# Optimization experiments

Hardware: AMD Instinct MI355X
Metric: run time of the kernel (lower is better)

## Reference

```python
import jax, jax.numpy as jnp
import numpy as np

B, S, V, CTX, NC, D, NH, L, FF, MAXS = 8, 512, 32000, 8, 512, 256, 4, 4, 512, 512
PAD = 0  # ram_model.pad_token_id


def setup_inputs() -> dict:
    key = jax.random.key(0)
    ks = iter(jax.random.split(key, 64))
    def p(shape, s=0.02):
        return jax.random.normal(next(ks), shape, jnp.float32) * s
    inp = {}
    inp["token_ids"] = jax.random.randint(next(ks), (B, S), 0, V)
    inp["ram_table"] = p((V, NC), 0.1)          # frozen RAM per-cluster scores
    inp["proj_W"] = p((NC, D)); inp["proj_b"] = jnp.zeros((D,), jnp.float32)
    inp["pos_emb"] = p((MAXS, D))
    for pre in ("sa", "ca"):
        for nm in ("Wq", "Wk", "Wv", "Wo"):
            inp[f"{pre}_{nm}"] = p((L, D, D))
        for nm in ("bq", "bk", "bv", "bo"):
            inp[f"{pre}_{nm}"] = jnp.zeros((L, D), jnp.float32)
    for i in (1, 2, 3):
        inp[f"ln{i}_s"] = jnp.ones((L, D), jnp.float32)
        inp[f"ln{i}_b"] = jnp.zeros((L, D), jnp.float32)
    inp["ff_W1"] = p((L, D, FF)); inp["ff_b1"] = jnp.zeros((L, FF), jnp.float32)
    inp["ff_W2"] = p((L, FF, D)); inp["ff_b2"] = jnp.zeros((L, D), jnp.float32)
    inp["out_W"] = p((D, V)); inp["out_b"] = jnp.zeros((V,), jnp.float32)
    return inp


def _ln(x, s, b):
    m = x.mean(-1, keepdims=True)
    v = ((x - m) ** 2).mean(-1, keepdims=True)
    return (x - m) * jax.lax.rsqrt(v + 1e-5) * s + b


def _mha(q_in, k_in, v_in, Wq, bq, Wk, bk, Wv, bv, Wo, bo, mask):
    b, sq, d = q_in.shape
    hd = d // NH
    q = (q_in @ Wq + bq).reshape(b, sq, NH, hd)
    k = (k_in @ Wk + bk).reshape(b, -1, NH, hd)
    v = (v_in @ Wv + bv).reshape(b, -1, NH, hd)
    sc = jnp.einsum("bqhd,bkhd->bhqk", q, k) / np.sqrt(hd).astype(np.float32)
    if mask is not None:
        sc = jnp.where(mask, -1e9, sc)  # mask broadcast over [b, h]
    a = jax.nn.softmax(sc, axis=-1)
    o = jnp.einsum("bhqk,bkhd->bqhd", a, v).reshape(b, sq, d)
    return o @ Wo + bo


def _forward(token_ids, ram_table, proj_W, proj_b, pos_emb,
             sa_Wq, sa_bq, sa_Wk, sa_bk, sa_Wv, sa_bv, sa_Wo, sa_bo,
             ca_Wq, ca_bq, ca_Wk, ca_bk, ca_Wv, ca_bv, ca_Wo, ca_bo,
             ln1_s, ln1_b, ln2_s, ln2_b, ln3_s, ln3_b,
             ff_W1, ff_b1, ff_W2, ff_b2, out_W, out_b):
    b, s = token_ids.shape
    # Batched sliding context windows (replaces the per-position Python loop):
    # left-pad with PAD so window at pos covers [pos-CTX+1, pos].
    padded = jnp.concatenate(
        [jnp.full((b, CTX - 1), PAD, token_ids.dtype), token_ids], axis=1)
    idx = jnp.arange(s)[:, None] + jnp.arange(CTX)[None, :]  # [S, CTX]
    win = padded[:, idx]                                      # [B, S, CTX]
    # Frozen RAM feature extraction: per-cluster scores averaged over window.
    scores = ram_table[win].mean(axis=2)                      # [B, S, NC]
    x = scores @ proj_W + proj_b + pos_emb[:s]                # [B, S, D]
    mask = jnp.triu(jnp.ones((s, s), bool), 1)                # causal
    mem = jnp.zeros((b, 1, D), x.dtype)
    for l in range(L):
        h = _ln(x, ln1_s[l], ln1_b[l])
        x = x + _mha(h, h, h, sa_Wq[l], sa_bq[l], sa_Wk[l], sa_bk[l],
                     sa_Wv[l], sa_bv[l], sa_Wo[l], sa_bo[l], mask)
        h = _ln(x, ln2_s[l], ln2_b[l])
        x = x + _mha(h, mem, mem, ca_Wq[l], ca_bq[l], ca_Wk[l], ca_bk[l],
                     ca_Wv[l], ca_bv[l], ca_Wo[l], ca_bo[l], None)
        h = _ln(x, ln3_s[l], ln3_b[l])
        x = x + jax.nn.relu(h @ ff_W1[l] + ff_b1[l]) @ ff_W2[l] + ff_b2[l]
    return x @ out_W + out_b                                  # [B, S, V]


def reference(token_ids, ram_table, proj_W, proj_b, pos_emb,
              sa_Wq, sa_bq, sa_Wk, sa_bk, sa_Wv, sa_bv, sa_Wo, sa_bo,
              ca_Wq, ca_bq, ca_Wk, ca_bk, ca_Wv, ca_bv, ca_Wo, ca_bo,
              ln1_s, ln1_b, ln2_s, ln2_b, ln3_s, ln3_b,
              ff_W1, ff_b1, ff_W2, ff_b2, out_W, out_b):
    return _forward(token_ids, ram_table, proj_W, proj_b, pos_emb,
                    sa_Wq, sa_bq, sa_Wk, sa_bk, sa_Wv, sa_bv, sa_Wo, sa_bo,
                    ca_Wq, ca_bq, ca_Wk, ca_bk, ca_Wv, ca_bv, ca_Wo, ca_bo,
                    ln1_s, ln1_b, ln2_s, ln2_b, ln3_s, ln3_b,
                    ff_W1, ff_b1, ff_W2, ff_b2, out_W, out_b)
```

## Files before the change

### kernel.cpp

```cpp
#include <hip/hip_runtime.h>

#define B_   8
#define S_   512
#define V_   32000
#define CTX_ 8
#define NC_  512
#define D_   256
#define NH_  4
#define L_   4
#define FF_  512
#define HD_  64
#define BS_  4096

#define FG_F32   1
#define FG_BF16  2
#define FG_RELU  4
#define FG_POS   8
#define FG_NT    16
#define FG_QKV   32

typedef __attribute__((ext_vector_type(8))) short bf16x8;
typedef __attribute__((ext_vector_type(4))) float f32x4;

__device__ inline void gload16(const void* g, void* lds) {
    __builtin_amdgcn_global_load_lds(
        (const __attribute__((address_space(1))) void*)g,
        (__attribute__((address_space(3))) void*)lds, 16, 0, 0);
}

__device__ inline ushort f2b(float f) {
    union { float f; unsigned u; } v; v.f = f;
    unsigned u = v.u;
    unsigned r = u + 0x7fffu + ((u >> 16) & 1u);
    return (ushort)(r >> 16);
}

__global__ __launch_bounds__(256) void prologue_kernel(
    const int* __restrict__ tok, const float* __restrict__ ram,
    const float* __restrict__ proj_W, const float* __restrict__ Wq,
    const float* __restrict__ Wk, const float* __restrict__ Wv,
    const float* __restrict__ Wo, const float* __restrict__ W1,
    const float* __restrict__ W2, const float* __restrict__ outW,
    const float* __restrict__ ca_bv, const float* __restrict__ ca_Wo,
    const float* __restrict__ ca_bo, const float* __restrict__ bq,
    const float* __restrict__ bk, const float* __restrict__ bv,
    ushort* __restrict__ pjWb, ushort* __restrict__ WqkvB,
    ushort* __restrict__ WoB, ushort* __restrict__ ff1B,
    ushort* __restrict__ ff2B, ushort* __restrict__ Wb,
    float* __restrict__ cc, float* __restrict__ qkvb,
    ushort* __restrict__ scores)
{
    __shared__ float tile[32 * 33];
    int id = blockIdx.x;
    int t = threadIdx.x;
    if (id < 10176) {
        const float* src; ushort* dst; int K, N, lt;
        if (id < 128)       { src = proj_W; dst = pjWb; K = 512; N = 256; lt = id; }
        else if (id < 896)  { lt = id - 128; int z = lt >> 6; lt &= 63;
                              int which = z / L_, l = z % L_;
                              src = (which == 0 ? Wq : which == 1 ? Wk : Wv) + (size_t)l * 65536;
                              dst = WqkvB + ((size_t)l * 768 + which * 256) * 256;
                              K = 256; N = 256; }
        else if (id < 1152) { lt = id - 896; int l = lt >> 6; lt &= 63;
                              src = Wo + (size_t)l * 65536; dst = WoB + (size_t)l * 65536;
                              K = 256; N = 256; }
        else if (id < 1664) { lt = id - 1152; int l = lt >> 7; lt &= 127;
                              src = W1 + (size_t)l * 131072; dst = ff1B + (size_t)l * 131072;
                              K = 256; N = 512; }
        else if (id < 2176) { lt = id - 1664; int l = lt >> 7; lt &= 127;
                              src = W2 + (size_t)l * 131072; dst = ff2B + (size_t)l * 131072;
                              K = 512; N = 256; }
        else                { lt = id - 2176; src = outW; dst = Wb; K = 256; N = 32000; }
        int ntc = N >> 5;
        int n0 = (lt % ntc) * 32, k0 = (lt / ntc) * 32;
        int tx = t & 31, ty = t >> 5;
        for (int i = ty; i < 32; i += 8)
            tile[i * 33 + tx] = src[(size_t)(k0 + i) * N + n0 + tx];
        __syncthreads();
        for (int i = ty; i < 32; i += 8)
            dst[(size_t)(n0 + i) * K + k0 + tx] = f2b(tile[tx * 33 + i]);
    } else if (id < 10180) {
        int l = id - 10176;
        const float* w = ca_Wo + (size_t)l * D_ * D_;
        const float* b = ca_bv + l * D_;
        float acc = 0.f;
        for (int d = 0; d < D_; ++d) acc += b[d] * w[(size_t)d * D_ + t];
        cc[l * D_ + t] = acc + ca_bo[l * D_ + t];
        for (int u = t; u < 768; u += 256) {
            int which = u >> 8, c = u & 255;
            const float* src = which == 0 ? bq : which == 1 ? bk : bv;
            qkvb[l * 768 + u] = src[l * 256 + c];
        }
    } else {
        int bs = id - 10180;
        int b = bs >> 9, s = bs & 511;
        float a0 = 0.f, a1 = 0.f;
        #pragma unroll
        for (int c = 0; c < CTX_; ++c) {
            int pos = s + c - (CTX_ - 1);
            int tk = (pos < 0) ? 0 : tok[b * S_ + pos];
            const float* row = ram + (size_t)tk * NC_;
            a0 += row[t];
            a1 += row[t + 256];
        }
        scores[(size_t)bs * NC_ + t]       = f2b(a0 * 0.125f);
        scores[(size_t)bs * NC_ + t + 256] = f2b(a1 * 0.125f);
    }
}

template<int K, int FLAGS>
__global__ __launch_bounds__(256) void gemm_row(
    const ushort* __restrict__ A, const ushort* __restrict__ Bt,
    const float* __restrict__ bias, const float* __restrict__ extra,
    const float* __restrict__ resid, const float* __restrict__ pos,
    const float* __restrict__ lnS, const float* __restrict__ lnB,
    float* __restrict__ Xout, ushort* __restrict__ Hout)
{
    __shared__ ushort As[16 * 64];
    __shared__ ushort Bs[256 * 64];
    __shared__ float red[2][4][16];
    int mt = blockIdx.x;
    int row0 = mt * 16;
    int t = threadIdx.x, w = t >> 6, lane = t & 63;
    int srow = lane >> 3, slot = lane & 7;
    int gcol = (slot ^ srow) * 8;
    int sl = lane >> 4, lc = lane & 15;
    int rA = lane & 15;

    f32x4 acc[4] = {};

    #pragma unroll
    for (int k0 = 0; k0 < K; k0 += 64) {
        if (w < 2)
            gload16(A + (size_t)(row0 + w * 8 + srow) * K + k0 + gcol, As + w * 512);
        #pragma unroll
        for (int c = 0; c < 8; ++c) {
            int chunk = w * 8 + c;
            gload16(Bt + (size_t)(chunk * 8 + srow) * K + k0 + gcol, Bs + chunk * 512);
        }
        __syncthreads();
        #pragma unroll
        for (int kk = 0; kk < 2; ++kk) {
            bf16x8 a = *reinterpret_cast<const bf16x8*>(
                As + rA * 64 + (((sl + kk * 4) ^ (rA & 7)) * 8));
            #pragma unroll
            for (int n = 0; n < 4; ++n) {
                int rr = w * 64 + (lane & 15) + n * 16;
                bf16x8 b = *reinterpret_cast<const bf16x8*>(
                    Bs + rr * 64 + (((sl + kk * 4) ^ (rr & 7)) * 8));
                acc[n] = __builtin_amdgcn_mfma_f32_16x16x32_bf16(a, b, acc[n], 0, 0, 0);
            }
        }
        __syncthreads();
    }

    float v[4][4];
    float psum[4] = {}, psq[4] = {};
    #pragma unroll
    for (int n = 0; n < 4; ++n) {
        int col = w * 64 + n * 16 + lc;
        float bn = bias[col];
        float en = extra ? extra[col] : 0.f;
        #pragma unroll
        for (int r = 0; r < 4; ++r) {
            int row = row0 + sl * 4 + r;
            float x = acc[n][r] + bn;
            if constexpr (FLAGS & FG_POS) x += pos[(size_t)(row & 511) * D_ + col];
            x += en;
            if (resid) x += resid[(size_t)row * D_ + col];
            v[n][r] = x;
            psum[r] += x;
            psq[r] += x * x;
        }
    }
    #pragma unroll
    for (int r = 0; r < 4; ++r) {
        #pragma unroll
        for (int o = 8; o > 0; o >>= 1) {
            psum[r] += __shfl_xor(psum[r], o);
            psq[r]  += __shfl_xor(psq[r], o);
        }
    }
    if (lc == 0) {
        #pragma unroll
        for (int r = 0; r < 4; ++r) {
            red[0][w][sl * 4 + r] = psum[r];
            red[1][w][sl * 4 + r] = psq[r];
        }
    }
    __syncthreads();
    #pragma unroll
    for (int r = 0; r < 4; ++r) {
        int rl = sl * 4 + r;
        float s  = red[0][0][rl] + red[0][1][rl] + red[0][2][rl] + red[0][3][rl];
        float s2 = red[1][0][rl] + red[1][1][rl] + red[1][2][rl] + red[1][3][rl];
        float mean = s * (1.f / D_);
        float var = s2 * (1.f / D_) - mean * mean;
        float rstd = rsqrtf(var + 1e-5f);
        int row = row0 + rl;
        #pragma unroll
        for (int n = 0; n < 4; ++n) {
            int col = w * 64 + n * 16 + lc;
            float x = v[n][r];
            Xout[(size_t)row * D_ + col] = x;
            Hout[(size_t)row * D_ + col] =
                f2b((x - mean) * rstd * lnS[col] + lnB[col]);
        }
    }
}

template<bool LAST>
__global__ __launch_bounds__(256) void ff_fused_kernel(
    const ushort* __restrict__ H, const ushort* __restrict__ W1t,
    const ushort* __restrict__ W2t, const float* __restrict__ b1,
    const float* __restrict__ b2, const float* __restrict__ xin,
    const float* __restrict__ lnS, const float* __restrict__ lnB,
    float* __restrict__ Xout, ushort* __restrict__ Hout,
    ushort* __restrict__ XBout)
{
    __shared__ ushort As[16 * 256];
    __shared__ ushort Bs1[64 * 256];
    __shared__ ushort Bs2[256 * 64];
    __shared__ ushort As2[16 * 64];
    __shared__ float red[2][4][16];
    int row0 = blockIdx.x * 16;
    int t = threadIdx.x, w = t >> 6, lane = t & 63;
    int srow = lane >> 3, slot = lane & 7;
    int gcol = (slot ^ srow) * 8;
    int sl = lane >> 4, lc = lane & 15;
    int rA = lane & 15;

    #pragma unroll
    for (int c = 0; c < 2; ++c) {
        int chunk = w * 2 + c;
        int ks = chunk >> 1, rbit = chunk & 1;
        gload16(H + (size_t)(row0 + rbit * 8 + srow) * 256 + ks * 64 + gcol,
                As + chunk * 512);
    }

    f32x4 xacc[4] = {};

    for (int c8 = 0; c8 < 8; ++c8) {
        int f0 = c8 * 64;
        #pragma unroll
        for (int c = 0; c < 8; ++c) {
            int chunk = w * 8 + c;
            int ks = chunk >> 3, rg = chunk & 7;
            gload16(W1t + (size_t)(f0 + rg * 8 + srow) * 256 + ks * 64 + gcol,
                    Bs1 + chunk * 512);
        }
        #pragma unroll
        for (int c = 0; c < 8; ++c) {
            int chunk = w * 8 + c;
            gload16(W2t + (size_t)(chunk * 8 + srow) * 512 + f0 + gcol,
                    Bs2 + chunk * 512);
        }
        __syncthreads();

        f32x4 a2 = {};
        #pragma unroll
        for (int ks = 0; ks < 4; ++ks) {
            #pragma unroll
            for (int kk = 0; kk < 2; ++kk) {
                bf16x8 a = *reinterpret_cast<const bf16x8*>(
                    As + ks * 1024 + rA * 64 + (((sl + kk * 4) ^ (rA & 7)) * 8));
                int rB = w * 16 + rA;
                bf16x8 b = *reinterpret_cast<const bf16x8*>(
                    Bs1 + ks * 4096 + rB * 64 + (((sl + kk * 4) ^ (rB & 7)) * 8));
                a2 = __builtin_amdgcn_mfma_f32_16x16x32_bf16(a, b, a2, 0, 0, 0);
            }
        }
        {
            float bn = b1[f0 + w * 16 + lc];
            #pragma unroll
            for (int r = 0; r < 4; ++r) {
                float p = fmaxf(a2[r] + bn, 0.f);
                int prow = sl * 4 + r;
                int pcol = w * 16 + lc;
                As2[prow * 64 + (((pcol >> 3) ^ (prow & 7)) * 8) + (pcol & 7)] = f2b(p);
            }
        }
        __syncthreads();
        #pragma unroll
        for (int kk = 0; kk < 2; ++kk) {
            bf16x8 a = *reinterpret_cast<const bf16x8*>(
                As2 + rA * 64 + (((sl + kk * 4) ^ (rA & 7)) * 8));
            #pragma unroll
            for (int n = 0; n < 4; ++n) {
                int rB = w * 64 + n * 16 + rA;
                bf16x8 b = *reinterpret_cast<const bf16x8*>(
                    Bs2 + rB * 64 + (((sl + kk * 4) ^ (rB & 7)) * 8));
                xacc[n] = __builtin_amdgcn_mfma_f32_16x16x32_bf16(a, b, xacc[n], 0, 0, 0);
            }
        }
        __syncthreads();
    }

    float v[4][4];
    float psum[4] = {}, psq[4] = {};
    #pragma unroll
    for (int n = 0; n < 4; ++n) {
        int col = w * 64 + n * 16 + lc;
        float bn = b2[col];
        #pragma unroll
        for (int r = 0; r < 4; ++r) {
            int row = row0 + sl * 4 + r;
            float x = xacc[n][r] + bn + xin[(size_t)row * D_ + col];
            v[n][r] = x;
            psum[r] += x;
            psq[r] += x * x;
        }
    }
    if constexpr (LAST) {
        #pragma unroll
        for (int n = 0; n < 4; ++n) {
            int col = w * 64 + n * 16 + lc;
            #pragma unroll
            for (int r = 0; r < 4; ++r) {
                int row = row0 + sl * 4 + r;
                XBout[(size_t)row * D_ + col] = f2b(v[n][r]);
            }
        }
        return;
    }
    #pragma unroll
    for (int r = 0; r < 4; ++r) {
        #pragma unroll
        for (int o = 8; o > 0; o >>= 1) {
            psum[r] += __shfl_xor(psum[r], o);
            psq[r]  += __shfl_xor(psq[r], o);
        }
    }
    if (lc == 0) {
        #pragma unroll
        for (int r = 0; r < 4; ++r) {
            red[0][w][sl * 4 + r] = psum[r];
            red[1][w][sl * 4 + r] = psq[r];
        }
    }
    __syncthreads();
    #pragma unroll
    for (int r = 0; r < 4; ++r) {
        int rl = sl * 4 + r;
        float s  = red[0][0][rl] + red[0][1][rl] + red[0][2][rl] + red[0][3][rl];
        float s2 = red[1][0][rl] + red[1][1][rl] + red[1][2][rl] + red[1][3][rl];
        float mean = s * (1.f / D_);
        float var = s2 * (1.f / D_) - mean * mean;
        float rstd = rsqrtf(var + 1e-5f);
        int row = row0 + rl;
        #pragma unroll
        for (int n = 0; n < 4; ++n) {
            int col = w * 64 + n * 16 + lc;
            float x = v[n][r];
            Xout[(size_t)row * D_ + col] = x;
            Hout[(size_t)row * D_ + col] =
                f2b((x - mean) * rstd * lnS[col] + lnB[col]);
        }
    }
}

template<int BM, int BN, int K, int TN, int FLAGS>
__global__ __launch_bounds__(256) void gemm_t(
    const ushort* __restrict__ A, const ushort* __restrict__ Bt,
    const float* __restrict__ bias, const float* __restrict__ extra,
    const float* __restrict__ resid, const float* __restrict__ pos,
    float* __restrict__ Cf, ushort* __restrict__ Cb)
{
    constexpr int WM = BM / 32;
    constexpr int WN = BN / 32;
    constexpr int MT = 4096 / BM;
    constexpr int NWG = MT * (TN / BN);
    __shared__ ushort smem[(BM + BN) * 64];
    ushort* As = smem;
    ushort* Bs = smem + BM * 64;
    int bid = blockIdx.x;
    int swz = bid;
    if constexpr ((NWG & 7) == 0) {
        constexpr int cpx = NWG >> 3;
        swz = (bid & 7) * cpx + (bid >> 3);
    }
    int mt = swz % MT, nt = swz / MT;
    int row0 = mt * BM, col0 = nt * BN;
    int t = threadIdx.x, w = t >> 6, lane = t & 63;
    int wr = w >> 1, wc = w & 1;
    int srow = lane >> 3, slot = lane & 7;
    int gcol = (slot ^ srow) * 8;

    f32x4 acc[WM][WN] = {};
    int sl = lane >> 4;
    int rA0 = wr * (BM / 2) + (lane & 15);
    int rB0 = wc * (BN / 2) + (lane & 15);

    #pragma unroll
    for (int k0 = 0; k0 < K; k0 += 64) {
        #pragma unroll
        for (int c = 0; c < BM / 32; ++c) {
            int chunk = w * (BM / 32) + c;
            gload16(A + (size_t)(row0 + chunk * 8 + srow) * K + k0 + gcol,
                    As + chunk * 512);
        }
        #pragma unroll
        for (int c = 0; c < BN / 32; ++c) {
            int chunk = w * (BN / 32) + c;
            gload16(Bt + (size_t)(col0 + chunk * 8 + srow) * K + k0 + gcol,
                    Bs + chunk * 512);
        }
        __syncthreads();
        #pragma unroll
        for (int kk = 0; kk < 2; ++kk) {
            bf16x8 a[WM], b[WN];
            #pragma unroll
            for (int m = 0; m < WM; ++m) {
                int rr = rA0 + m * 16;
                a[m] = *reinterpret_cast<const bf16x8*>(
                    As + rr * 64 + (((sl + kk * 4) ^ (rr & 7)) * 8));
            }
            #pragma unroll
            for (int n = 0; n < WN; ++n) {
                int rr = rB0 + n * 16;
                b[n] = *reinterpret_cast<const bf16x8*>(
                    Bs + rr * 64 + (((sl + kk * 4) ^ (rr & 7)) * 8));
            }
            #pragma unroll
            for (int m = 0; m < WM; ++m)
                #pragma unroll
                for (int n = 0; n < WN; ++n)
                    acc[m][n] = __builtin_amdgcn_mfma_f32_16x16x32_bf16(
                        a[m], b[n], acc[m][n], 0, 0, 0);
        }
        __syncthreads();
    }

    int lr = (lane >> 4) * 4;
    int lc = lane & 15;

    if constexpr (FLAGS & FG_NT) {
        float* Ct = reinterpret_cast<float*>(smem);
        #pragma unroll
        for (int p = 0; p < 2; ++p) {
            __syncthreads();
            if (wr == p) {
                #pragma unroll
                for (int n = 0; n < WN; ++n) {
                    int colL = wc * (BN / 2) + n * 16 + lc;
                    float bn = bias[col0 + colL];
                    #pragma unroll
                    for (int m = 0; m < WM; ++m)
                        #pragma unroll
                        for (int r = 0; r < 4; ++r)
                            Ct[(m * 16 + lr + r) * BN + colL] = acc[m][n][r] + bn;
                }
            }
            __syncthreads();
            constexpr int NV4 = (BM / 2) * (BN / 4);
            #pragma unroll
            for (int j = 0; j < NV4 / 256; ++j) {
                int idx = t + j * 256;
                int rl = idx / (BN / 4);
                int c4 = idx % (BN / 4);
                f32x4 v4 = reinterpret_cast<const f32x4*>(Ct)[idx];
                __builtin_nontemporal_store(v4,
                    reinterpret_cast<f32x4*>(
                        &Cf[(size_t)(row0 + p * (BM / 2) + rl) * TN + col0 + c4 * 4]));
            }
        }
        return;
    }

    #pragma unroll
    for (int n = 0; n < WN; ++n) {
        int col = col0 + wc * (BN / 2) + n * 16 + lc;
        float bn = bias ? bias[col] : 0.f;
        float en = extra ? extra[col] : 0.f;
        #pragma unroll
        for (int m = 0; m < WM; ++m) {
            int rbase = row0 + wr * (BM / 2) + m * 16 + lr;
            #pragma unroll
            for (int r = 0; r < 4; ++r) {
                int row = rbase + r;
                float v = acc[m][n][r] + bn;
                if constexpr (FLAGS & FG_QKV) {
                    int which = col >> 8;
                    int c2 = col & 255;
                    int hh = c2 >> 6, dd = c2 & 63;
                    int bb = row >> 9, ss = row & 511;
                    if (which == 0) {
                        Cb[((((size_t)bb * NH_ + hh) * S_ + ss) << 6) + dd] =
                            f2b(v * 0.125f);
                    } else if (which == 1) {
                        (Cb + 1048576)[((((size_t)bb * NH_ + hh) * S_ + ss) << 6) + dd] =
                            f2b(v);
                    } else {
                        (Cb + 2097152)[((((size_t)bb * NH_ + hh) * HD_ + dd) << 9) + ss] =
                            f2b(v);
                    }
                } else {
                    if constexpr (FLAGS & FG_POS) v += pos[(size_t)(row & 511) * TN + col];
                    if (extra) v += en;
                    if (resid) v += resid[(size_t)row * TN + col];
                    if constexpr (FLAGS & FG_RELU) v = fmaxf(v, 0.f);
                    if constexpr (FLAGS & FG_BF16)
                        Cb[(size_t)row * TN + col] = f2b(v);
                    if constexpr (FLAGS & FG_F32)
                        Cf[(size_t)row * TN + col] = v;
                }
            }
        }
    }
}

__global__ __launch_bounds__(256) void attn_kernel(
    const ushort* __restrict__ q, const ushort* __restrict__ k,
    const ushort* __restrict__ vT, ushort* __restrict__ pv)
{
    int qt = blockIdx.x, bh = blockIdx.y;
    __shared__ ushort smem[20480];
    ushort* Ps = smem + 16384;
    int t = threadIdx.x, w = t >> 6, lane = t & 63;
    int srow = lane >> 3, slot = lane & 7;
    int gcol = (slot ^ srow) * 8;
    int sl = lane >> 4, lc = lane & 15;

    const ushort* Qp = q + ((size_t)bh * S_ + qt * 64) * HD_;
    const ushort* Kp = k + (size_t)bh * S_ * HD_;
    const ushort* Vp = vT + (size_t)bh * HD_ * S_;

    int qrow = w * 16 + lc;
    bf16x8 qf0 = *reinterpret_cast<const bf16x8*>(Qp + qrow * 64 + sl * 8);
    bf16x8 qf1 = *reinterpret_cast<const bf16x8*>(Qp + qrow * 64 + sl * 8 + 32);

    f32x4 o[4] = {};
    float m_r[4], l_r[4];
    #pragma unroll
    for (int r = 0; r < 4; ++r) { m_r[r] = -1e30f; l_r[r] = 0.f; }
    int row_abs = qt * 64 + w * 16 + sl * 4;

    {
        ushort* Ks = smem;
        ushort* Vs = smem + 4096;
        #pragma unroll
        for (int c = 0; c < 2; ++c) {
            int chunk = w * 2 + c;
            gload16(Kp + (size_t)(chunk * 8 + srow) * 64 + gcol, Ks + chunk * 512);
            gload16(Vp + (size_t)(chunk * 8 + srow) * 512 + gcol, Vs + chunk * 512);
        }
    }

    for (int kt = 0; kt <= qt; ++kt) {
        int cur = kt & 1;
        ushort* Ks = smem + cur * 8192;
        ushort* Vs = smem + cur * 8192 + 4096;
        __syncthreads();
        if (kt < qt) {
            ushort* Kn = smem + (cur ^ 1) * 8192;
            ushort* Vn = Kn + 4096;
            #pragma unroll
            for (int c = 0; c < 2; ++c) {
                int chunk = w * 2 + c;
                gload16(Kp + (size_t)((kt + 1) * 64 + chunk * 8 + srow) * 64 + gcol,
                        Kn + chunk * 512);
                gload16(Vp + (size_t)(chunk * 8 + srow) * 512 + (kt + 1) * 64 + gcol,
                        Vn + chunk * 512);
            }
        }

        f32x4 sa[4] = {};
        #pragma unroll
        for (int n = 0; n < 4; ++n) {
            int rB = n * 16 + lc;
            bf16x8 b0 = *reinterpret_cast<const bf16x8*>(
                Ks + rB * 64 + ((sl ^ (rB & 7)) * 8));
            bf16x8 b1 = *reinterpret_cast<const bf16x8*>(
                Ks + rB * 64 + (((sl + 4) ^ (rB & 7)) * 8));
            sa[n] = __builtin_amdgcn_mfma_f32_16x16x32_bf16(qf0, b0, sa[n], 0, 0, 0);
            sa[n] = __builtin_amdgcn_mfma_f32_16x16x32_bf16(qf1, b1, sa[n], 0, 0, 0);
        }
        if (kt == qt) {
            #pragma unroll
            for (int n = 0; n < 4; ++n) {
                int col = kt * 64 + n * 16 + lc;
                #pragma unroll
                for (int r = 0; r < 4; ++r)
                    if (col > row_abs + r) sa[n][r] = -1e30f;
            }
        }
        float psum[4];
        #pragma unroll
        for (int r = 0; r < 4; ++r) {
            float vm = fmaxf(fmaxf(sa[0][r], sa[1][r]), fmaxf(sa[2][r], sa[3][r]));
            vm = fmaxf(vm, __shfl_xor(vm, 1));
            vm = fmaxf(vm, __shfl_xor(vm, 2));
            vm = fmaxf(vm, __shfl_xor(vm, 4));
            vm = fmaxf(vm, __shfl_xor(vm, 8));
            float mn = fmaxf(m_r[r], vm);
            float scl = __expf(m_r[r] - mn);
            m_r[r] = mn;
            l_r[r] *= scl;
            #pragma unroll
            for (int n = 0; n < 4; ++n) o[n][r] *= scl;
            psum[r] = 0.f;
        }
        ushort* Pw = Ps + w * 1024;
        #pragma unroll
        for (int n = 0; n < 4; ++n) {
            #pragma unroll
            for (int r = 0; r < 4; ++r) {
                float p = __expf(sa[n][r] - m_r[r]);
                psum[r] += p;
                int prow = sl * 4 + r;
                int pcol = n * 16 + lc;
                int pslot = pcol >> 3;
                Pw[prow * 64 + ((pslot ^ (prow & 7)) * 8) + (pcol & 7)] = f2b(p);
            }
        }
        #pragma unroll
        for (int r = 0; r < 4; ++r) {
            float s = psum[r];
            s += __shfl_xor(s, 1);
            s += __shfl_xor(s, 2);
            s += __shfl_xor(s, 4);
            s += __shfl_xor(s, 8);
            l_r[r] += s;
        }
        int arow = lc;
        bf16x8 pa0 = *reinterpret_cast<const bf16x8*>(
            Pw + arow * 64 + ((sl ^ (arow & 7)) * 8));
        bf16x8 pa1 = *reinterpret_cast<const bf16x8*>(
            Pw + arow * 64 + (((sl + 4) ^ (arow & 7)) * 8));
        #pragma unroll
        for (int n = 0; n < 4; ++n) {
            int rB = n * 16 + lc;
            bf16x8 v0 = *reinterpret_cast<const bf16x8*>(
                Vs + rB * 64 + ((sl ^ (rB & 7)) * 8));
            bf16x8 v1 = *reinterpret_cast<const bf16x8*>(
                Vs + rB * 64 + (((sl + 4) ^ (rB & 7)) * 8));
            o[n] = __builtin_amdgcn_mfma_f32_16x16x32_bf16(pa0, v0, o[n], 0, 0, 0);
            o[n] = __builtin_amdgcn_mfma_f32_16x16x32_bf16(pa1, v1, o[n], 0, 0, 0);
        }
    }

    int bb = bh >> 2, hh = bh & 3;
    #pragma unroll
    for (int r = 0; r < 4; ++r) {
        float inv = 1.f / l_r[r];
        int ss = qt * 64 + w * 16 + sl * 4 + r;
        #pragma unroll
        for (int n = 0; n < 4; ++n) {
            int dd = n * 16 + lc;
            pv[((size_t)bb * S_ + ss) * D_ + hh * HD_ + dd] = f2b(o[n][r] * inv);
        }
    }
}

extern "C" void kernel_launch(void* const* d_in, const int* in_sizes, int n_in,
                              void* d_out, int out_size, void* d_ws, size_t ws_size,
                              hipStream_t stream)
{
    const int*   tok     = (const int*)  d_in[0];
    const float* ram     = (const float*)d_in[1];
    const float* proj_W  = (const float*)d_in[2];
    const float* proj_b  = (const float*)d_in[3];
    const float* pos_emb = (const float*)d_in[4];
    const float* sa_Wq   = (const float*)d_in[5];
    const float* sa_Wk   = (const float*)d_in[6];
    const float* sa_Wv   = (const float*)d_in[7];
    const float* sa_Wo   = (const float*)d_in[8];
    const float* sa_bq   = (const float*)d_in[9];
    const float* sa_bk   = (const float*)d_in[10];
    const float* sa_bv   = (const float*)d_in[11];
    const float* sa_bo   = (const float*)d_in[12];
    const float* ca_Wo   = (const float*)d_in[16];
    const float* ca_bv   = (const float*)d_in[19];
    const float* ca_bo   = (const float*)d_in[20];
    const float* ln1_s   = (const float*)d_in[21];
    const float* ln1_b   = (const float*)d_in[22];
    const float* ln3_s   = (const float*)d_in[25];
    const float* ln3_b   = (const float*)d_in[26];
    const float* ff_W1   = (const float*)d_in[27];
    const float* ff_b1   = (const float*)d_in[28];
    const float* ff_W2   = (const float*)d_in[29];
    const float* ff_b2   = (const float*)d_in[30];
    const float* out_W   = (const float*)d_in[31];
    const float* out_b   = (const float*)d_in[32];

    float* out = (float*)d_out;
    float* ws  = (float*)d_ws;

    float*  x   = ws;
    float*  cc  = ws + (size_t)BS_ * D_;
    ushort* xb  = (ushort*)(cc + L_ * D_);
    ushort* Wb  = xb + (size_t)BS_ * D_;

    ushort* sc_b  = (ushort*)out;
    ushort* h_b   = sc_b + 2097152;
    ushort* qkv3  = h_b + 1048576;
    ushort* pv_b  = qkv3 + 3145728;
    ushort* pjWb  = pv_b + 1048576;
    ushort* WqkvB = pjWb + 131072;
    ushort* WoB   = WqkvB + 786432;
    ushort* ff1B  = WoB + 262144;
    ushort* ff2B  = ff1B + 524288;
    float*  qkvb  = (float*)(ff2B + 524288);
    ushort* qb_b  = qkv3;
    ushort* kb_b  = qkv3 + 1048576;
    ushort* vT_b  = qkv3 + 2097152;

    prologue_kernel<<<14276, 256, 0, stream>>>(
        tok, ram, proj_W, sa_Wq, sa_Wk, sa_Wv, sa_Wo, ff_W1, ff_W2, out_W,
        ca_bv, ca_Wo, ca_bo, sa_bq, sa_bk, sa_bv,
        pjWb, WqkvB, WoB, ff1B, ff2B, Wb, cc, qkvb, sc_b);

    gemm_row<512, FG_POS><<<256, 256, 0, stream>>>(
        sc_b, pjWb, proj_b, nullptr, nullptr, pos_emb,
        ln1_s, ln1_b, x, h_b);

    for (int l = 0; l < L_; ++l) {
        gemm_t<64, 64, 256, 768, FG_QKV><<<768, 256, 0, stream>>>(
            h_b, WqkvB + (size_t)l * 196608, qkvb + l * 768,
            nullptr, nullptr, nullptr, nullptr, qkv3);
        attn_kernel<<<dim3(8, 32), 256, 0, stream>>>(qb_b, kb_b, vT_b, pv_b);
        gemm_row<256, 0><<<256, 256, 0, stream>>>(
            pv_b, WoB + (size_t)l * 65536, sa_bo + l * D_,
            cc + l * D_, x, nullptr, ln3_s + l * D_, ln3_b + l * D_, x, h_b);
        if (l < L_ - 1) {
            ff_fused_kernel<false><<<256, 256, 0, stream>>>(
                h_b, ff1B + (size_t)l * 131072, ff2B + (size_t)l * 131072,
                ff_b1 + l * FF_, ff_b2 + l * D_, x,
                ln1_s + (l + 1) * D_, ln1_b + (l + 1) * D_, x, h_b, nullptr);
        } else {
            ff_fused_kernel<true><<<256, 256, 0, stream>>>(
                h_b, ff1B + (size_t)l * 131072, ff2B + (size_t)l * 131072,
                ff_b1 + l * FF_, ff_b2 + l * D_, x,
                nullptr, nullptr, nullptr, nullptr, xb);
        }
    }

    gemm_t<128, 128, 256, 32000, FG_F32 | FG_NT><<<8000, 256, 0, stream>>>(
        xb, Wb, out_b, nullptr, nullptr, nullptr, out, nullptr);
}
```

Baseline: 380.1 us.

## Fuse attention output projection and LayerNorm into the feed-forward kernel

The self-attention output projection (Wo GEMM plus bias, cross-attention constant and residual), LayerNorm3, and the feed-forward block now run in one kernel per 16-row tile. The normalized activations stay in LDS and the residual stays in registers, so the intermediate x/h round trip through global memory and one launch per layer go away. In exchange the kernel uses more LDS and does more serial work per block with only 256 blocks, which may lower occupancy.

```diff
diff --git a/kernel.cpp b/kernel.cpp
--- a/kernel.cpp
+++ b/kernel.cpp
@@ -210,15 +210,19 @@
 }
 
 template<bool LAST>
-__global__ __launch_bounds__(256) void ff_fused_kernel(
-    const ushort* __restrict__ H, const ushort* __restrict__ W1t,
-    const ushort* __restrict__ W2t, const float* __restrict__ b1,
-    const float* __restrict__ b2, const float* __restrict__ xin,
-    const float* __restrict__ lnS, const float* __restrict__ lnB,
+__global__ __launch_bounds__(256) void tail_fused_kernel(
+    const ushort* __restrict__ pv, const ushort* __restrict__ WoT,
+    const float* __restrict__ bo, const float* __restrict__ ccl,
+    const float* __restrict__ xin,
+    const float* __restrict__ ln3S, const float* __restrict__ ln3B,
+    const ushort* __restrict__ W1t, const ushort* __restrict__ W2t,
+    const float* __restrict__ b1, const float* __restrict__ b2,
+    const float* __restrict__ ln1S, const float* __restrict__ ln1B,
     float* __restrict__ Xout, ushort* __restrict__ Hout,
     ushort* __restrict__ XBout)
 {
-    __shared__ ushort As[16 * 256];
+    __shared__ ushort Ah[16 * 256];
+    __shared__ ushort As1[16 * 64];
     __shared__ ushort Bs1[64 * 256];
     __shared__ ushort Bs2[256 * 64];
     __shared__ ushort As2[16 * 64];
@@ -230,16 +234,85 @@
     int sl = lane >> 4, lc = lane & 15;
     int rA = lane & 15;
 
-    #pragma unroll
-    for (int c = 0; c < 2; ++c) {
-        int chunk = w * 2 + c;
-        int ks = chunk >> 1, rbit = chunk & 1;
-        gload16(H + (size_t)(row0 + rbit * 8 + srow) * 256 + ks * 64 + gcol,
-                As + chunk * 512);
-    }
+    f32x4 acc[4] = {};
+    #pragma unroll
+    for (int k0 = 0; k0 < 256; k0 += 64) {
+        if (w < 2)
+            gload16(pv + (size_t)(row0 + w * 8 + srow) * 256 + k0 + gcol, As1 + w * 512);
+        #pragma unroll
+        for (int c = 0; c < 8; ++c) {
+            int chunk = w * 8 + c;
+            gload16(WoT + (size_t)(chunk * 8 + srow) * 256 + k0 + gcol, Bs2 + chunk * 512);
+        }
+        __syncthreads();
+        #pragma unroll
+        for (int kk = 0; kk < 2; ++kk) {
+            bf16x8 a = *reinterpret_cast<const bf16x8*>(
+                As1 + rA * 64 + (((sl + kk * 4) ^ (rA & 7)) * 8));
+            #pragma unroll
+            for (int n = 0; n < 4; ++n) {
+                int rr = w * 64 + rA + n * 16;
+                bf16x8 b = *reinterpret_cast<const bf16x8*>(
+                    Bs2 + rr * 64 + (((sl + kk * 4) ^ (rr & 7)) * 8));
+                acc[n] = __builtin_amdgcn_mfma_f32_16x16x32_bf16(a, b, acc[n], 0, 0, 0);
+            }
+        }
+        __syncthreads();
+    }
+
+    float v[4][4];
+    {
+        float psum[4] = {}, psq[4] = {};
+        #pragma unroll
+        for (int n = 0; n < 4; ++n) {
+            int col = w * 64 + n * 16 + lc;
+            float bn = bo[col] + ccl[col];
+            #pragma unroll
+            for (int r = 0; r < 4; ++r) {
+                int row = row0 + sl * 4 + r;
+                float x = acc[n][r] + bn + xin[(size_t)row * D_ + col];
+                v[n][r] = x;
+                psum[r] += x;
+                psq[r] += x * x;
+            }
+        }
+        #pragma unroll
+        for (int r = 0; r < 4; ++r) {
+            #pragma unroll
+            for (int o = 8; o > 0; o >>= 1) {
+                psum[r] += __shfl_xor(psum[r], o);
+                psq[r]  += __shfl_xor(psq[r], o);
+            }
+        }
+        if (lc == 0) {
+            #pragma unroll
+            for (int r = 0; r < 4; ++r) {
+                red[0][w][sl * 4 + r] = psum[r];
+                red[1][w][sl * 4 + r] = psq[r];
+            }
+        }
+        __syncthreads();
+        #pragma unroll
+        for (int r = 0; r < 4; ++r) {
+            int rl = sl * 4 + r;
+            float s  = red[0][0][rl] + red[0][1][rl] + red[0][2][rl] + red[0][3][rl];
+            float s2 = red[1][0][rl] + red[1][1][rl] + red[1][2][rl] + red[1][3][rl];
+            float mean = s * (1.f / D_);
+            float var = s2 * (1.f / D_) - mean * mean;
+            float rstd = rsqrtf(var + 1e-5f);
+            #pragma unroll
+            for (int n = 0; n < 4; ++n) {
+                int col = w * 64 + n * 16 + lc;
+                int colk = n * 16 + lc;
+                float h = (v[n][r] - mean) * rstd * ln3S[col] + ln3B[col];
+                Ah[w * 1024 + rl * 64 + (((colk >> 3) ^ (rl & 7)) * 8) + (colk & 7)] =
+                    f2b(h);
+            }
+        }
+    }
+    __syncthreads();
 
     f32x4 xacc[4] = {};
-
     for (int c8 = 0; c8 < 8; ++c8) {
         int f0 = c8 * 64;
         #pragma unroll
@@ -263,7 +336,7 @@
             #pragma unroll
             for (int kk = 0; kk < 2; ++kk) {
                 bf16x8 a = *reinterpret_cast<const bf16x8*>(
-                    As + ks * 1024 + rA * 64 + (((sl + kk * 4) ^ (rA & 7)) * 8));
+                    Ah + ks * 1024 + rA * 64 + (((sl + kk * 4) ^ (rA & 7)) * 8));
                 int rB = w * 16 + rA;
                 bf16x8 b = *reinterpret_cast<const bf16x8*>(
                     Bs1 + ks * 4096 + rB * 64 + (((sl + kk * 4) ^ (rB & 7)) * 8));
@@ -296,7 +369,6 @@
         __syncthreads();
     }
 
-    float v[4][4];
     float psum[4] = {}, psq[4] = {};
     #pragma unroll
     for (int n = 0; n < 4; ++n) {
@@ -304,8 +376,7 @@
         float bn = b2[col];
         #pragma unroll
         for (int r = 0; r < 4; ++r) {
-            int row = row0 + sl * 4 + r;
-            float x = xacc[n][r] + bn + xin[(size_t)row * D_ + col];
+            float x = xacc[n][r] + bn + v[n][r];
             v[n][r] = x;
             psum[r] += x;
             psq[r] += x * x;
@@ -354,7 +425,7 @@
             float x = v[n][r];
             Xout[(size_t)row * D_ + col] = x;
             Hout[(size_t)row * D_ + col] =
-                f2b((x - mean) * rstd * lnS[col] + lnB[col]);
+                f2b((x - mean) * rstd * ln1S[col] + ln1B[col]);
         }
     }
 }
@@ -719,18 +790,19 @@
             h_b, WqkvB + (size_t)l * 196608, qkvb + l * 768,
             nullptr, nullptr, nullptr, nullptr, qkv3);
         attn_kernel<<<dim3(8, 32), 256, 0, stream>>>(qb_b, kb_b, vT_b, pv_b);
-        gemm_row<256, 0><<<256, 256, 0, stream>>>(
-            pv_b, WoB + (size_t)l * 65536, sa_bo + l * D_,
-            cc + l * D_, x, nullptr, ln3_s + l * D_, ln3_b + l * D_, x, h_b);
         if (l < L_ - 1) {
-            ff_fused_kernel<false><<<256, 256, 0, stream>>>(
-                h_b, ff1B + (size_t)l * 131072, ff2B + (size_t)l * 131072,
-                ff_b1 + l * FF_, ff_b2 + l * D_, x,
+            tail_fused_kernel<false><<<256, 256, 0, stream>>>(
+                pv_b, WoB + (size_t)l * 65536, sa_bo + l * D_, cc + l * D_, x,
+                ln3_s + l * D_, ln3_b + l * D_,
+                ff1B + (size_t)l * 131072, ff2B + (size_t)l * 131072,
+                ff_b1 + l * FF_, ff_b2 + l * D_,
                 ln1_s + (l + 1) * D_, ln1_b + (l + 1) * D_, x, h_b, nullptr);
         } else {
-            ff_fused_kernel<true><<<256, 256, 0, stream>>>(
-                h_b, ff1B + (size_t)l * 131072, ff2B + (size_t)l * 131072,
-                ff_b1 + l * FF_, ff_b2 + l * D_, x,
+            tail_fused_kernel<true><<<256, 256, 0, stream>>>(
+                pv_b, WoB + (size_t)l * 65536, sa_bo + l * D_, cc + l * D_, x,
+                ln3_s + l * D_, ln3_b + l * D_,
+                ff1B + (size_t)l * 131072, ff2B + (size_t)l * 131072,
+                ff_b1 + l * FF_, ff_b2 + l * D_,
                 nullptr, nullptr, nullptr, nullptr, xb);
         }
     }
```

After: 350.4 us, median of 2. 1.08x faster.
